# Kernel optimization log

Hardware: AMD Instinct MI355X
Metric: run time of the kernel (lower is better)

The kernel has to match this reference:

```python
import jax, jax.numpy as jnp
import numpy as np

DIM = 512
NUM_HEADS = 8
HEAD_DIM = DIM // NUM_HEADS
SCALE = HEAD_DIM ** -0.5


def setup_inputs() -> dict:
    key = jax.random.key(0)
    ks = jax.random.split(key, 6)
    B, N = 2, 4096
    x = jax.random.normal(ks[0], (B, N, DIM), dtype=jnp.float32)
    # xavier_uniform for qkv [3*dim, dim] and proj [dim, dim] (torch Linear weight layout [out,in])
    lim_qkv = float(np.sqrt(6.0 / (3 * DIM + DIM)))
    w_qkv = jax.random.uniform(ks[1], (3 * DIM, DIM), minval=-lim_qkv, maxval=lim_qkv, dtype=jnp.float32)
    lim_p = float(np.sqrt(6.0 / (DIM + DIM)))
    w_proj = jax.random.uniform(ks[2], (DIM, DIM), minval=-lim_p, maxval=lim_p, dtype=jnp.float32)
    b_proj = jnp.zeros((DIM,), dtype=jnp.float32)
    ln_gamma = jnp.ones((DIM,), dtype=jnp.float32)
    ln_beta = jnp.zeros((DIM,), dtype=jnp.float32)
    return {"x": x, "w_qkv": w_qkv, "w_proj": w_proj, "b_proj": b_proj,
            "ln_gamma": ln_gamma, "ln_beta": ln_beta}


def _attention(x, w_qkv, w_proj, b_proj, ln_gamma, ln_beta):
    B, N, C = x.shape
    qkv = jnp.einsum('bnc,dc->bnd', x, w_qkv)              # [B,N,3C]
    qkv = qkv.reshape(B, N, 3, NUM_HEADS, HEAD_DIM)
    qkv = jnp.transpose(qkv, (2, 0, 3, 1, 4))              # [3,B,H,N,Dh]
    q, k, v = qkv[0], qkv[1], qkv[2]
    attn = jnp.einsum('bhnd,bhmd->bhnm', q, k) * SCALE     # [B,H,N,N]
    attn = jax.nn.softmax(attn, axis=-1)
    # dropout is identity in eval mode
    out = jnp.einsum('bhnm,bhmd->bhnd', attn, v)           # [B,H,N,Dh]
    out = jnp.transpose(out, (0, 2, 1, 3)).reshape(B, N, C)
    out = jnp.einsum('bnc,dc->bnd', out, w_proj) + b_proj
    y = x + out
    mean = jnp.mean(y, axis=-1, keepdims=True)
    var = jnp.var(y, axis=-1, keepdims=True)
    return (y - mean) / jnp.sqrt(var + 1e-5) * ln_gamma + ln_beta


def reference(x, w_qkv, w_proj, b_proj, ln_gamma, ln_beta):
    return _attention(x, w_qkv, w_proj, b_proj, ln_gamma, ln_beta)
```

## Files before the change

### kernel.cpp

```cpp
#include <hip/hip_runtime.h>
#include <hip/hip_bf16.h>

#define SEQ    4096
#define CDIM   512
#define NHEADS 8
#define HDIM   64
#define QSCALE 0.18033688f

typedef __attribute__((ext_vector_type(4))) float f32x4;
typedef __attribute__((ext_vector_type(8))) short bf16x8;

__device__ __forceinline__ int swz(int row, int col) {
    int b = (row << 7) + (col << 1);
    b ^= (row & 7) << 4;
    return b >> 1;
}

__device__ __forceinline__ short f2bf(float f) {
    union { __hip_bfloat16 h; short s; } u;
    u.h = __float2bfloat16(f);
    return u.s;
}

__device__ __forceinline__ void gl16(const void* g, void* l) {
    __builtin_amdgcn_global_load_lds(
        (const __attribute__((address_space(1))) unsigned int*)g,
        (__attribute__((address_space(3))) unsigned int*)l,
        16, 0, 0);
}

__global__ __launch_bounds__(256) void cvt_k(
    const float* __restrict__ a, short* __restrict__ o, int n4)
{
    int i = blockIdx.x * 256 + threadIdx.x;
    const int stride = gridDim.x * 256;
    for (; i < n4; i += stride) {
        float4 v = ((const float4*)a)[i];
        short4 r;
        r.x = f2bf(v.x); r.y = f2bf(v.y); r.z = f2bf(v.z); r.w = f2bf(v.w);
        ((short4*)o)[i] = r;
    }
}

__global__ __launch_bounds__(256) void qkv_gemm_k(
    const short* __restrict__ xb, const short* __restrict__ wb,
    short* __restrict__ qb, short* __restrict__ kb, short* __restrict__ vtb)
{
    __shared__ alignas(16) short As[2][128 * 64];
    __shared__ alignas(16) short Bs[2][128 * 64];
    const int tid  = threadIdx.x;
    const int lane = tid & 63;
    const int l15  = lane & 15;
    const int lg   = lane >> 4;
    const int wv   = tid >> 6;
    const int wy   = wv >> 1, wx = wv & 1;
    const int m0 = blockIdx.x * 128;
    const int n0 = blockIdx.y * 128;

    const f32x4 fzero = {0.f, 0.f, 0.f, 0.f};
    f32x4 acc[4][4];
    #pragma unroll
    for (int i = 0; i < 4; ++i)
        #pragma unroll
        for (int j = 0; j < 4; ++j)
            acc[i][j] = fzero;

    const int row0 = wv * 8 + (lane >> 3);
    const int cb   = ((lane & 7) ^ (lane >> 3)) << 4;
    const char* agp = (const char*)xb + (size_t)(m0 + row0) * 1024 + cb;
    const char* bgp = (const char*)wb + (size_t)(n0 + row0) * 1024 + cb;
    char* al0 = (char*)&As[0][0] + wv * 1024;
    char* al1 = (char*)&As[1][0] + wv * 1024;
    char* bl0 = (char*)&Bs[0][0] + wv * 1024;
    char* bl1 = (char*)&Bs[1][0] + wv * 1024;

    #define QSTAGE(al, bl, kofs) do {                                  \
        _Pragma("unroll")                                              \
        for (int i_ = 0; i_ < 4; ++i_) {                               \
            gl16(agp + (kofs) + i_ * 32768, (al) + i_ * 4096);         \
            gl16(bgp + (kofs) + i_ * 32768, (bl) + i_ * 4096);         \
        } } while (0)

    QSTAGE(al0, bl0, 0);

    int cur = 0;
    for (int k0 = 0; k0 < CDIM; k0 += 64) {
        asm volatile("s_waitcnt vmcnt(0)" ::: "memory");
        __syncthreads();
        if (k0 + 64 < CDIM) {
            if (cur == 0) QSTAGE(al1, bl1, (k0 + 64) * 2);
            else          QSTAGE(al0, bl0, (k0 + 64) * 2);
        }
        const short* Ac = cur ? &As[1][0] : &As[0][0];
        const short* Bc = cur ? &Bs[1][0] : &Bs[0][0];

        #pragma unroll
        for (int ks = 0; ks < 2; ++ks) {
            bf16x8 afr[4], bfr[4];
            #pragma unroll
            for (int i = 0; i < 4; ++i) {
                afr[i] = *(const bf16x8*)(&Ac[swz(wy * 64 + i * 16 + l15, ks * 32 + lg * 8)]);
                bfr[i] = *(const bf16x8*)(&Bc[swz(wx * 64 + i * 16 + l15, ks * 32 + lg * 8)]);
            }
            #pragma unroll
            for (int i = 0; i < 4; ++i)
                #pragma unroll
                for (int j = 0; j < 4; ++j)
                    acc[i][j] = __builtin_amdgcn_mfma_f32_16x16x32_bf16(afr[i], bfr[j], acc[i][j], 0, 0, 0);
        }
        cur ^= 1;
    }
    #undef QSTAGE

    #pragma unroll
    for (int j = 0; j < 4; ++j) {
        const int d = n0 + wx * 64 + j * 16 + l15;
        const int s = d >> 9;
        const int h = (d >> 6) & 7;
        const int e = d & 63;
        #pragma unroll
        for (int i = 0; i < 4; ++i) {
            #pragma unroll
            for (int r = 0; r < 4; ++r) {
                const int m  = m0 + wy * 64 + i * 16 + lg * 4 + r;
                const int bb = m >> 12;
                const int n  = m & (SEQ - 1);
                const int bh = bb * NHEADS + h;
                const float v = acc[i][j][r];
                if (s == 0) {
                    qb[(((size_t)bh * SEQ + n) << 6) + e] = f2bf(v * QSCALE);
                } else if (s == 1) {
                    kb[(((size_t)bh * SEQ + n) << 6) + e] = f2bf(v);
                } else {
                    const int c  = n & 63;
                    const int cp = (c & 0x23) | ((c & 0x0C) << 1) | ((c & 0x10) >> 2);
                    vtb[((size_t)bh << 18) + ((size_t)(n >> 6) << 12) + (e << 6) + cp] = f2bf(v);
                }
            }
        }
    }
}

__global__ __launch_bounds__(512) void attn_k(
    const short* __restrict__ qb, const short* __restrict__ kb, const short* __restrict__ vtb,
    short* __restrict__ ob)
{
    __shared__ alignas(16) char smem[81920];
    const int tid  = threadIdx.x;
    const int lane = tid & 63;
    const int l15  = lane & 15;
    const int lg   = lane >> 4;
    const int wv   = (tid >> 6) & 3;
    const int wg   = tid >> 8;
    const int lin  = blockIdx.x;
    const int bh   = lin & 15;
    const int q0   = (lin >> 4) << 7;
    const int b    = bh >> 3, h = bh & 7;
    const size_t base = (size_t)bh * SEQ * HDIM;

    bf16x8 qf[2][2];
    #pragma unroll
    for (int qi = 0; qi < 2; ++qi) {
        const short* qp = qb + base + (size_t)(q0 + wv * 32 + qi * 16 + l15) * HDIM + lg * 8;
        qf[qi][0] = *(const bf16x8*)(qp);
        qf[qi][1] = *(const bf16x8*)(qp + 32);
    }

    const f32x4 fzero = {0.f, 0.f, 0.f, 0.f};
    f32x4 acc[2][4];
    f32x4 lacc[2];
    #pragma unroll
    for (int qi = 0; qi < 2; ++qi) {
        lacc[qi] = fzero;
        #pragma unroll
        for (int di = 0; di < 4; ++di) acc[qi][di] = fzero;
    }

    bf16x8 ones;
    #pragma unroll
    for (int e = 0; e < 8; ++e) ones[e] = (short)0x3F80;

    const int t0  = wv * 128 + lane;
    const int cbs = ((t0 & 7) ^ ((t0 >> 3) & 7)) << 4;
    const int ghb = wg * 262144;
    const char* kgp = (const char*)(kb + base) + ghb + (((t0 >> 3) << 7) + cbs);
    const char* vgp = (const char*)(vtb + ((size_t)bh << 18)) + ghb + (((t0 >> 3) << 7) + cbs);
    char* const gb = smem + wg * 40960;
    char* K0p = gb +     0 + wv * 2048;  const short* Kr0 = (const short*)(gb);
    char* K1p = gb +  8192 + wv * 2048;  const short* Kr1 = (const short*)(gb + 8192);
    char* V0p = gb + 16384 + wv * 2048;  const short* Vr0 = (const short*)(gb + 16384);
    char* V1p = gb + 24576 + wv * 2048;  const short* Vr1 = (const short*)(gb + 24576);
    char* V2p = gb + 32768 + wv * 2048;  const short* Vr2 = (const short*)(gb + 32768);

    bf16x8 paA[2][2], paB[2][2];

    #define STAGE(klp, vlp, TI) do {                                       \
        _Pragma("unroll")                                                  \
        for (int i_ = 0; i_ < 2; ++i_) {                                   \
            gl16(kgp + (TI) * 8192 + i_ * 1024, (klp) + i_ * 1024);        \
            gl16(vgp + (TI) * 8192 + i_ * 1024, (vlp) + i_ * 1024);        \
        } } while (0)

    #define MFMA16(a_, b_, c_) __builtin_amdgcn_mfma_f32_16x16x32_bf16(a_, b_, c_, 0, 0, 0)

    #define BODY(TILE, KRD, VPR, KSTP, VSTP, PAP, PAN, DOSTG) do {             \
        asm volatile("s_waitcnt vmcnt(0)" ::: "memory");                       \
        __syncthreads();                                                       \
        if (DOSTG) { STAGE(KSTP, VSTP, (TILE) + 1); }                          \
        _Pragma("unroll")                                                      \
        for (int ni = 0; ni < 4; ++ni) {                                       \
            bf16x8 kf0 = *(const bf16x8*)(&(KRD)[swz(ni * 16 + l15, lg * 8)]);      \
            bf16x8 kf1 = *(const bf16x8*)(&(KRD)[swz(ni * 16 + l15, 32 + lg * 8)]); \
            f32x4 s0 = fzero, s1 = fzero;                                      \
            s0 = MFMA16(kf0, qf[0][0], s0);                                    \
            s0 = MFMA16(kf1, qf[0][1], s0);                                    \
            s1 = MFMA16(kf0, qf[1][0], s1);                                    \
            s1 = MFMA16(kf1, qf[1][1], s1);                                    \
            bf16x8 v0 = *(const bf16x8*)(&(VPR)[swz(ni * 16 + l15, lg * 8)]);       \
            bf16x8 v1 = *(const bf16x8*)(&(VPR)[swz(ni * 16 + l15, 32 + lg * 8)]);  \
            acc[0][ni] = MFMA16(PAP[0][0], v0, acc[0][ni]);                    \
            acc[0][ni] = MFMA16(PAP[0][1], v1, acc[0][ni]);                    \
            acc[1][ni] = MFMA16(PAP[1][0], v0, acc[1][ni]);                    \
            acc[1][ni] = MFMA16(PAP[1][1], v1, acc[1][ni]);                    \
            if (ni == 0) { lacc[0] = MFMA16(PAP[0][0], ones, lacc[0]);         \
                           lacc[0] = MFMA16(PAP[0][1], ones, lacc[0]); }       \
            if (ni == 1) { lacc[1] = MFMA16(PAP[1][0], ones, lacc[1]);         \
                           lacc[1] = MFMA16(PAP[1][1], ones, lacc[1]); }       \
            _Pragma("unroll")                                                  \
            for (int r = 0; r < 4; ++r) {                                      \
                PAN[0][ni >> 1][(ni & 1) * 4 + r] = f2bf(__builtin_amdgcn_exp2f(s0[r])); \
                PAN[1][ni >> 1][(ni & 1) * 4 + r] = f2bf(__builtin_amdgcn_exp2f(s1[r])); \
            }                                                                  \
        }                                                                      \
    } while (0)

    STAGE(K0p, V0p, 0);
    asm volatile("s_waitcnt vmcnt(0)" ::: "memory");
    __syncthreads();
    STAGE(K1p, V1p, 1);
    #pragma unroll
    for (int ni = 0; ni < 4; ++ni) {
        bf16x8 kf0 = *(const bf16x8*)(&Kr0[swz(ni * 16 + l15, lg * 8)]);
        bf16x8 kf1 = *(const bf16x8*)(&Kr0[swz(ni * 16 + l15, 32 + lg * 8)]);
        f32x4 s0 = fzero, s1 = fzero;
        s0 = MFMA16(kf0, qf[0][0], s0);
        s0 = MFMA16(kf1, qf[0][1], s0);
        s1 = MFMA16(kf0, qf[1][0], s1);
        s1 = MFMA16(kf1, qf[1][1], s1);
        #pragma unroll
        for (int r = 0; r < 4; ++r) {
            paA[0][ni >> 1][(ni & 1) * 4 + r] = f2bf(__builtin_amdgcn_exp2f(s0[r]));
            paA[1][ni >> 1][(ni & 1) * 4 + r] = f2bf(__builtin_amdgcn_exp2f(s1[r]));
        }
    }

    for (int i = 0; i < 5; ++i) {
        BODY(6 * i + 1, Kr1, Vr0, K0p, V2p, paA, paB, 1);
        BODY(6 * i + 2, Kr0, Vr1, K1p, V0p, paB, paA, 1);
        BODY(6 * i + 3, Kr1, Vr2, K0p, V1p, paA, paB, 1);
        BODY(6 * i + 4, Kr0, Vr0, K1p, V2p, paB, paA, 1);
        BODY(6 * i + 5, Kr1, Vr1, K0p, V0p, paA, paB, 1);
        BODY(6 * i + 6, Kr0, Vr2, K1p, V1p, paB, paA, 1);
    }
    BODY(31, Kr1, Vr0, K0p, V2p, paA, paB, 0);

    #pragma unroll
    for (int dd = 0; dd < 4; ++dd) {
        bf16x8 v0 = *(const bf16x8*)(&Vr1[swz(dd * 16 + l15, lg * 8)]);
        bf16x8 v1 = *(const bf16x8*)(&Vr1[swz(dd * 16 + l15, 32 + lg * 8)]);
        acc[0][dd] = MFMA16(paB[0][0], v0, acc[0][dd]);
        acc[0][dd] = MFMA16(paB[0][1], v1, acc[0][dd]);
        acc[1][dd] = MFMA16(paB[1][0], v0, acc[1][dd]);
        acc[1][dd] = MFMA16(paB[1][1], v1, acc[1][dd]);
    }
    lacc[0] = MFMA16(paB[0][0], ones, lacc[0]);
    lacc[0] = MFMA16(paB[0][1], ones, lacc[0]);
    lacc[1] = MFMA16(paB[1][0], ones, lacc[1]);
    lacc[1] = MFMA16(paB[1][1], ones, lacc[1]);
    #undef BODY
    #undef MFMA16
    #undef STAGE

    __syncthreads();
    float* xch = (float*)smem;
    const int xi = (wv * 64 + lane) * 44;
    if (wg == 1) {
        #pragma unroll
        for (int qi = 0; qi < 2; ++qi) {
            #pragma unroll
            for (int di = 0; di < 4; ++di)
                *(f32x4*)(xch + xi + qi * 16 + di * 4) = acc[qi][di];
            *(f32x4*)(xch + xi + 32 + qi * 4) = lacc[qi];
        }
    }
    __syncthreads();
    if (wg == 0) {
        #pragma unroll
        for (int qi = 0; qi < 2; ++qi) {
            #pragma unroll
            for (int di = 0; di < 4; ++di)
                acc[qi][di] += *(const f32x4*)(xch + xi + qi * 16 + di * 4);
            lacc[qi] += *(const f32x4*)(xch + xi + 32 + qi * 4);
        }
        #pragma unroll
        for (int qi = 0; qi < 2; ++qi) {
            float inv[4];
            #pragma unroll
            for (int r = 0; r < 4; ++r) inv[r] = 1.0f / lacc[qi][r];
            #pragma unroll
            for (int di = 0; di < 4; ++di) {
                const int e = di * 16 + l15;
                #pragma unroll
                for (int r = 0; r < 4; ++r) {
                    const int qn = q0 + wv * 32 + qi * 16 + lg * 4 + r;
                    ob[((size_t)(b * SEQ + qn) << 9) + h * 64 + e] = f2bf(acc[qi][di][r] * inv[r]);
                }
            }
        }
    }
}

__global__ __launch_bounds__(256) void proj_k(
    const short* __restrict__ ao, const short* __restrict__ wpb,
    const float* __restrict__ bp, const float* __restrict__ x,
    float* __restrict__ y)
{
    __shared__ alignas(16) short As[2][128 * 64];
    __shared__ alignas(16) short Bs[2][128 * 64];
    const int tid  = threadIdx.x;
    const int lane = tid & 63;
    const int l15  = lane & 15;
    const int lg   = lane >> 4;
    const int wv   = tid >> 6;
    const int wy   = wv >> 1, wx = wv & 1;
    const int m0 = blockIdx.x * 128;
    const int n0 = blockIdx.y * 128;

    const f32x4 fzero = {0.f, 0.f, 0.f, 0.f};
    f32x4 acc[4][4];
    #pragma unroll
    for (int i = 0; i < 4; ++i)
        #pragma unroll
        for (int j = 0; j < 4; ++j)
            acc[i][j] = fzero;

    const int row0 = wv * 8 + (lane >> 3);
    const int cb   = ((lane & 7) ^ (lane >> 3)) << 4;
    const char* agp = (const char*)ao  + (size_t)(m0 + row0) * 1024 + cb;
    const char* bgp = (const char*)wpb + (size_t)(n0 + row0) * 1024 + cb;
    char* al0 = (char*)&As[0][0] + wv * 1024;
    char* al1 = (char*)&As[1][0] + wv * 1024;
    char* bl0 = (char*)&Bs[0][0] + wv * 1024;
    char* bl1 = (char*)&Bs[1][0] + wv * 1024;

    #define PSTAGE(al, bl, kofs) do {                                  \
        _Pragma("unroll")                                              \
        for (int i_ = 0; i_ < 4; ++i_) {                               \
            gl16(agp + (kofs) + i_ * 32768, (al) + i_ * 4096);         \
            gl16(bgp + (kofs) + i_ * 32768, (bl) + i_ * 4096);         \
        } } while (0)

    PSTAGE(al0, bl0, 0);

    int cur = 0;
    for (int k0 = 0; k0 < CDIM; k0 += 64) {
        asm volatile("s_waitcnt vmcnt(0)" ::: "memory");
        __syncthreads();
        if (k0 + 64 < CDIM) {
            if (cur == 0) PSTAGE(al1, bl1, (k0 + 64) * 2);
            else          PSTAGE(al0, bl0, (k0 + 64) * 2);
        }
        const short* Ac = cur ? &As[1][0] : &As[0][0];
        const short* Bc = cur ? &Bs[1][0] : &Bs[0][0];

        #pragma unroll
        for (int ks = 0; ks < 2; ++ks) {
            bf16x8 afr[4], bfr[4];
            #pragma unroll
            for (int i = 0; i < 4; ++i) {
                afr[i] = *(const bf16x8*)(&Ac[swz(wy * 64 + i * 16 + l15, ks * 32 + lg * 8)]);
                bfr[i] = *(const bf16x8*)(&Bc[swz(wx * 64 + i * 16 + l15, ks * 32 + lg * 8)]);
            }
            #pragma unroll
            for (int i = 0; i < 4; ++i)
                #pragma unroll
                for (int j = 0; j < 4; ++j)
                    acc[i][j] = __builtin_amdgcn_mfma_f32_16x16x32_bf16(afr[i], bfr[j], acc[i][j], 0, 0, 0);
        }
        cur ^= 1;
    }
    #undef PSTAGE

    #pragma unroll
    for (int i = 0; i < 4; ++i) {
        #pragma unroll
        for (int j = 0; j < 4; ++j) {
            const int d = n0 + wx * 64 + j * 16 + l15;
            #pragma unroll
            for (int r = 0; r < 4; ++r) {
                const int m = m0 + wy * 64 + i * 16 + lg * 4 + r;
                const size_t idx = (size_t)m * CDIM + d;
                y[idx] = acc[i][j][r] + bp[d] + x[idx];
            }
        }
    }
}

__global__ __launch_bounds__(256) void ln_k(
    float* __restrict__ y, const float* __restrict__ gm, const float* __restrict__ bt)
{
    const int lane = threadIdx.x & 63;
    const int row  = blockIdx.x * 4 + (threadIdx.x >> 6);
    float* p = y + (size_t)row * CDIM;
    float4 a = *(const float4*)(p + lane * 4);
    float4 b = *(const float4*)(p + 256 + lane * 4);
    float s = a.x + a.y + a.z + a.w + b.x + b.y + b.z + b.w;
    float q = a.x * a.x + a.y * a.y + a.z * a.z + a.w * a.w
            + b.x * b.x + b.y * b.y + b.z * b.z + b.w * b.w;
    #pragma unroll
    for (int mm = 1; mm < 64; mm <<= 1) {
        s += __shfl_xor(s, mm, 64);
        q += __shfl_xor(q, mm, 64);
    }
    const float mean = s * (1.0f / CDIM);
    const float var  = q * (1.0f / CDIM) - mean * mean;
    const float inv  = rsqrtf(var + 1e-5f);
    float4 g0 = *(const float4*)(gm + lane * 4);
    float4 g1 = *(const float4*)(gm + 256 + lane * 4);
    float4 t0 = *(const float4*)(bt + lane * 4);
    float4 t1 = *(const float4*)(bt + 256 + lane * 4);
    float4 r0, r1;
    r0.x = (a.x - mean) * inv * g0.x + t0.x;
    r0.y = (a.y - mean) * inv * g0.y + t0.y;
    r0.z = (a.z - mean) * inv * g0.z + t0.z;
    r0.w = (a.w - mean) * inv * g0.w + t0.w;
    r1.x = (b.x - mean) * inv * g1.x + t1.x;
    r1.y = (b.y - mean) * inv * g1.y + t1.y;
    r1.z = (b.z - mean) * inv * g1.z + t1.z;
    r1.w = (b.w - mean) * inv * g1.w + t1.w;
    *(float4*)(p + lane * 4) = r0;
    *(float4*)(p + 256 + lane * 4) = r1;
}

extern "C" void kernel_launch(void* const* d_in, const int* in_sizes, int n_in,
                              void* d_out, int out_size, void* d_ws, size_t ws_size,
                              hipStream_t stream)
{
    const float* x      = (const float*)d_in[0];
    const float* w_qkv  = (const float*)d_in[1];
    const float* w_proj = (const float*)d_in[2];
    const float* b_proj = (const float*)d_in[3];
    const float* gamma  = (const float*)d_in[4];
    const float* beta   = (const float*)d_in[5];
    float* out = (float*)d_out;

    const size_t qkv_elems = (size_t)16 * SEQ * HDIM;
    short* qb    = (short*)d_ws;
    short* kb    = qb + qkv_elems;
    short* vtb   = kb + qkv_elems;
    short* ob    = vtb + qkv_elems;
    short* xb    = ob;
    short* wqkvb = ob + qkv_elems;
    short* wpb   = qb;

    cvt_k     <<<dim3(1024),   256, 0, stream>>>(x, xb, (2 * SEQ * CDIM) / 4);
    cvt_k     <<<dim3(256),    256, 0, stream>>>(w_qkv, wqkvb, (3 * CDIM * CDIM) / 4);
    qkv_gemm_k<<<dim3(64, 12), 256, 0, stream>>>(xb, wqkvb, qb, kb, vtb);
    attn_k    <<<dim3(512),    512, 0, stream>>>(qb, kb, vtb, ob);
    cvt_k     <<<dim3(256),    256, 0, stream>>>(w_proj, wpb, (CDIM * CDIM) / 4);
    proj_k    <<<dim3(64, 4),  256, 0, stream>>>(ob, wpb, b_proj, x, out);
    ln_k      <<<dim3(2048),   256, 0, stream>>>(out, gamma, beta);
}
```

Measured before the change: 121.9 us.

## Merge three bf16 conversions into one launch and stagger attention KV tile order

The three fp32-to-bf16 conversion kernels (x, w_qkv, w_proj) are merged into one launch. The w_proj conversion moves out from between attention and projection, and its buffer moves to a separate workspace region. In the attention kernel, the second half of the blocks start their KV tile loop at a rotated offset (phase 16), so concurrent blocks read different K/V tiles and contend less for the same memory lines. The rotation is safe because softmax is taken without max subtraction and the per-tile sums commute, but the merged conversion kernel now does per-element branching to pick its source.

New measurement: 117.5 us. 3.6% less time.

```diff
diff --git a/kernel.cpp b/kernel.cpp
--- a/kernel.cpp
+++ b/kernel.cpp
@@ -29,16 +29,23 @@
         16, 0, 0);
 }
 
-__global__ __launch_bounds__(256) void cvt_k(
-    const float* __restrict__ a, short* __restrict__ o, int n4)
-{
+__global__ __launch_bounds__(256) void cvt3_k(
+    const float* __restrict__ a0, short* __restrict__ o0, int c0,
+    const float* __restrict__ a1, short* __restrict__ o1, int c1,
+    const float* __restrict__ a2, short* __restrict__ o2, int c2)
+{
+    const int total = c0 + c1 + c2;
     int i = blockIdx.x * 256 + threadIdx.x;
     const int stride = gridDim.x * 256;
-    for (; i < n4; i += stride) {
-        float4 v = ((const float4*)a)[i];
+    for (; i < total; i += stride) {
+        const float* a; short* o; int j;
+        if (i < c0)           { a = a0; o = o0; j = i; }
+        else if (i < c0 + c1) { a = a1; o = o1; j = i - c0; }
+        else                  { a = a2; o = o2; j = i - c0 - c1; }
+        float4 v = ((const float4*)a)[j];
         short4 r;
         r.x = f2bf(v.x); r.y = f2bf(v.y); r.z = f2bf(v.z); r.w = f2bf(v.w);
-        ((short4*)o)[i] = r;
+        ((short4*)o)[j] = r;
     }
 }
 
@@ -156,6 +163,7 @@
     const int bh   = lin & 15;
     const int q0   = (lin >> 4) << 7;
     const int b    = bh >> 3, h = bh & 7;
+    const int phase = ((lin >> 8) & 1) << 4;
     const size_t base = (size_t)bh * SEQ * HDIM;
 
     bf16x8 qf[2][2];
@@ -194,11 +202,13 @@
 
     bf16x8 paA[2][2], paB[2][2];
 
-    #define STAGE(klp, vlp, TI) do {                                       \
+    #define TOFS(T) (((phase + (T)) & 31) * 8192)
+
+    #define STAGE(klp, vlp, BOFS) do {                                     \
         _Pragma("unroll")                                                  \
         for (int i_ = 0; i_ < 2; ++i_) {                                   \
-            gl16(kgp + (TI) * 8192 + i_ * 1024, (klp) + i_ * 1024);        \
-            gl16(vgp + (TI) * 8192 + i_ * 1024, (vlp) + i_ * 1024);        \
+            gl16(kgp + (BOFS) + i_ * 1024, (klp) + i_ * 1024);             \
+            gl16(vgp + (BOFS) + i_ * 1024, (vlp) + i_ * 1024);             \
         } } while (0)
 
     #define MFMA16(a_, b_, c_) __builtin_amdgcn_mfma_f32_16x16x32_bf16(a_, b_, c_, 0, 0, 0)
@@ -206,7 +216,7 @@
     #define BODY(TILE, KRD, VPR, KSTP, VSTP, PAP, PAN, DOSTG) do {             \
         asm volatile("s_waitcnt vmcnt(0)" ::: "memory");                       \
         __syncthreads();                                                       \
-        if (DOSTG) { STAGE(KSTP, VSTP, (TILE) + 1); }                          \
+        if (DOSTG) { STAGE(KSTP, VSTP, TOFS((TILE) + 1)); }                    \
         _Pragma("unroll")                                                      \
         for (int ni = 0; ni < 4; ++ni) {                                       \
             bf16x8 kf0 = *(const bf16x8*)(&(KRD)[swz(ni * 16 + l15, lg * 8)]);      \
@@ -234,10 +244,10 @@
         }                                                                      \
     } while (0)
 
-    STAGE(K0p, V0p, 0);
+    STAGE(K0p, V0p, TOFS(0));
     asm volatile("s_waitcnt vmcnt(0)" ::: "memory");
     __syncthreads();
-    STAGE(K1p, V1p, 1);
+    STAGE(K1p, V1p, TOFS(1));
     #pragma unroll
     for (int ni = 0; ni < 4; ++ni) {
         bf16x8 kf0 = *(const bf16x8*)(&Kr0[swz(ni * 16 + l15, lg * 8)]);
@@ -280,6 +290,7 @@
     #undef BODY
     #undef MFMA16
     #undef STAGE
+    #undef TOFS
 
     __syncthreads();
     float* xch = (float*)smem;
@@ -461,13 +472,14 @@
     short* ob    = vtb + qkv_elems;
     short* xb    = ob;
     short* wqkvb = ob + qkv_elems;
-    short* wpb   = qb;
-
-    cvt_k     <<<dim3(1024),   256, 0, stream>>>(x, xb, (2 * SEQ * CDIM) / 4);
-    cvt_k     <<<dim3(256),    256, 0, stream>>>(w_qkv, wqkvb, (3 * CDIM * CDIM) / 4);
+    short* wpb   = wqkvb + (size_t)3 * CDIM * CDIM;
+
+    cvt3_k    <<<dim3(1024),   256, 0, stream>>>(
+        x, xb, (2 * SEQ * CDIM) / 4,
+        w_qkv, wqkvb, (3 * CDIM * CDIM) / 4,
+        w_proj, wpb, (CDIM * CDIM) / 4);
     qkv_gemm_k<<<dim3(64, 12), 256, 0, stream>>>(xb, wqkvb, qb, kb, vtb);
     attn_k    <<<dim3(512),    512, 0, stream>>>(qb, kb, vtb, ob);
-    cvt_k     <<<dim3(256),    256, 0, stream>>>(w_proj, wpb, (CDIM * CDIM) / 4);
     proj_k    <<<dim3(64, 4),  256, 0, stream>>>(ob, wpb, b_proj, x, out);
     ln_k      <<<dim3(2048),   256, 0, stream>>>(out, gamma, beta);
 }
```
